# Kernel optimization log

Hardware: AMD Instinct MI355X
Metric: run time of the kernel (lower is better)

## Reference

```python
import jax, jax.numpy as jnp
import numpy as np

NEG_INF = -1e30


def setup_inputs() -> dict:
    key = jax.random.key(0)
    k1, k2, k3, k4, k5, k6 = jax.random.split(key, 6)
    T, B = 256, 8
    Din, Dm, A = 256, 256, 128
    input = jax.random.normal(k1, (T, B, Din), dtype=jnp.float32)
    memory = jax.random.normal(k2, (T, B, Dm), dtype=jnp.float32)
    memory_mask = jax.random.randint(k3, (T, B), 0, 2, dtype=jnp.int32)
    # first Linear weight [A, Din+Dm] split into input / memory halves (additive decomposition)
    scale1 = 1.0 / np.sqrt(Din + Dm)
    Wi = jax.random.uniform(k4, (Din, A), minval=-scale1, maxval=scale1, dtype=jnp.float32)
    Wm = jax.random.uniform(k5, (Dm, A), minval=-scale1, maxval=scale1, dtype=jnp.float32)
    # second Linear weight [1, A] -> vector [A]
    scale2 = 1.0 / np.sqrt(A)
    v = jax.random.uniform(k6, (A,), minval=-scale2, maxval=scale2, dtype=jnp.float32)
    return {"input": input, "memory": memory, "memory_mask": memory_mask,
            "Wi": Wi, "Wm": Wm, "v": v}


def reference(input, memory, memory_mask, Wi, Wm, v):
    # input: [T, B, Din], memory: [T, B, Dm], memory_mask: [T, B]
    # Additive (Bahdanau) scores: v . tanh(Wi x_s + Wm m_t). Concat+Linear on
    # [x; m] with block weight [Wi; Wm] equals the sum of the two projections.
    ip = jnp.einsum('tbd,da->tba', input, Wi)[:, None]    # [T, 1, B, A]
    mp = jnp.einsum('tbd,da->tba', memory, Wm)[None]      # [1, T, B, A]
    logits = jnp.einsum('stba,a->stb', jnp.tanh(ip + mp), v)  # [T, T, B]
    masked = jnp.where(memory_mask[None] != 0, logits, NEG_INF)
    score = jax.nn.softmax(masked, axis=1)                # softmax over key dim
    # NOTE: original module weights `input` (not memory) as values.
    context = jnp.einsum('stb,tbd->sbd', score, input)    # [T, B, Din]
    return jnp.concatenate([context, input], axis=-1)      # [T, B, 2*Din]
```

## Files before the change

### kernel.cpp

```cpp
#include <hip/hip_runtime.h>

#define T_DIM 256
#define B_DIM 8
#define DIN   256
#define DM    256
#define A_DIM 128
#define S_TILE 4
#define NEG_INF_F (-1e30f)

__global__ __launch_bounds__(256) void proj_kernel(
    const float* __restrict__ input, const float* __restrict__ memory,
    const float* __restrict__ Wi, const float* __restrict__ Wm,
    float* __restrict__ IP, float* __restrict__ MPt)
{
    __shared__ float xin[DIN];
    __shared__ float xmem[DM];
    const int tb  = blockIdx.x;
    const int t   = tb / B_DIM;
    const int b   = tb % B_DIM;
    const int tid = threadIdx.x;

    xin[tid]  = input[(t * B_DIM + b) * DIN + tid];
    xmem[tid] = memory[(t * B_DIM + b) * DM + tid];
    __syncthreads();

    if (tid < A_DIM) {
        const int a = tid;
        float acc = 0.f;
        #pragma unroll 8
        for (int d = 0; d < DIN; ++d)
            acc = fmaf(xin[d], Wi[d * A_DIM + a], acc);
        IP[(t * B_DIM + b) * A_DIM + a] = acc;
    } else {
        const int a = tid - A_DIM;
        float acc = 0.f;
        #pragma unroll 8
        for (int d = 0; d < DM; ++d)
            acc = fmaf(xmem[d], Wm[d * A_DIM + a], acc);
        MPt[(b * A_DIM + a) * T_DIM + t] = acc;
    }
}

__device__ inline float warp_red_max(float v) {
    #pragma unroll
    for (int o = 32; o > 0; o >>= 1) v = fmaxf(v, __shfl_xor(v, o, 64));
    return v;
}
__device__ inline float warp_red_sum(float v) {
    #pragma unroll
    for (int o = 32; o > 0; o >>= 1) v += __shfl_xor(v, o, 64);
    return v;
}

__global__ __launch_bounds__(256) void attn_kernel(
    const float* __restrict__ input, const int* __restrict__ mask,
    const float* __restrict__ v, const float* __restrict__ IP,
    const float* __restrict__ MPt, float* __restrict__ out)
{
    __shared__ float ip_s[S_TILE][A_DIM];
    __shared__ float vs[A_DIM];
    __shared__ float sc[S_TILE][T_DIM];
    __shared__ float red[4];

    const int blk = blockIdx.x;
    const int b   = blk % B_DIM;
    const int s0  = (blk / B_DIM) * S_TILE;
    const int tid = threadIdx.x;
    const int lane = tid & 63;
    const int wave = tid >> 6;

    if (tid < A_DIM) vs[tid] = v[tid];
    for (int i = tid; i < S_TILE * A_DIM; i += 256) {
        const int s = i / A_DIM, a = i % A_DIM;
        ip_s[s][a] = IP[((s0 + s) * B_DIM + b) * A_DIM + a];
    }
    __syncthreads();

    const int t = tid;
    float acc[S_TILE];
    #pragma unroll
    for (int s = 0; s < S_TILE; ++s) acc[s] = 0.f;

    const float* mp_base = MPt + (size_t)(b * A_DIM) * T_DIM + t;
    #pragma unroll 4
    for (int a = 0; a < A_DIM; ++a) {
        const float mp = mp_base[(size_t)a * T_DIM];
        const float va = vs[a];
        #pragma unroll
        for (int s = 0; s < S_TILE; ++s) {
            const float x = ip_s[s][a] + mp;
            const float e  = __expf(2.f * x);
            const float th = fmaf(-2.f, __builtin_amdgcn_rcpf(e + 1.f), 1.f);
            acc[s] = fmaf(va, th, acc[s]);
        }
    }

    const bool valid = (mask[t * B_DIM + b] != 0);

    #pragma unroll
    for (int s = 0; s < S_TILE; ++s) {
        const float masked = valid ? acc[s] : NEG_INF_F;
        float wm = warp_red_max(masked);
        if (lane == 0) red[wave] = wm;
        __syncthreads();
        const float m = fmaxf(fmaxf(red[0], red[1]), fmaxf(red[2], red[3]));
        const float e = __expf(masked - m);
        float ws = warp_red_sum(e);
        __syncthreads();
        if (lane == 0) red[wave] = ws;
        __syncthreads();
        const float sum = red[0] + red[1] + red[2] + red[3];
        sc[s][t] = e * __builtin_amdgcn_rcpf(sum);
        __syncthreads();
    }

    const int d = tid;
    float ctx[S_TILE];
    #pragma unroll
    for (int s = 0; s < S_TILE; ++s) ctx[s] = 0.f;

    #pragma unroll 4
    for (int t2 = 0; t2 < T_DIM; ++t2) {
        const float xv = input[(t2 * B_DIM + b) * DIN + d];
        #pragma unroll
        for (int s = 0; s < S_TILE; ++s)
            ctx[s] = fmaf(sc[s][t2], xv, ctx[s]);
    }

    #pragma unroll
    for (int s = 0; s < S_TILE; ++s) {
        const int srow = s0 + s;
        out[((size_t)(srow * B_DIM + b)) * (2 * DIN) + d]       = ctx[s];
        out[((size_t)(srow * B_DIM + b)) * (2 * DIN) + DIN + d] = input[(srow * B_DIM + b) * DIN + d];
    }
}

extern "C" void kernel_launch(void* const* d_in, const int* in_sizes, int n_in,
                              void* d_out, int out_size, void* d_ws, size_t ws_size,
                              hipStream_t stream) {
    const float* input  = (const float*)d_in[0];
    const float* memory = (const float*)d_in[1];
    const int*   mask   = (const int*)d_in[2];
    const float* Wi     = (const float*)d_in[3];
    const float* Wm     = (const float*)d_in[4];
    const float* v      = (const float*)d_in[5];
    float* out = (float*)d_out;

    float* IP  = (float*)d_ws;
    float* MPt = IP + (size_t)T_DIM * B_DIM * A_DIM;

    proj_kernel<<<T_DIM * B_DIM, 256, 0, stream>>>(input, memory, Wi, Wm, IP, MPt);
    attn_kernel<<<(T_DIM / S_TILE) * B_DIM, 256, 0, stream>>>(input, mask, v, IP, MPt, out);
}
```

Measured before the change: 116.4 us.

## Fold tanh scaling into projections and halve query tile

Pre-scales both projections by 2*log2(e) so the inner loop computes tanh through a raw exp2 and a reciprocal. The tanh constant terms are folded out of the loop: the sum of v times one is a per-row constant that cancels in the softmax, and the factor -2 is applied once to the logits. S_TILE drops from 4 to 2, which doubles the block count and merges the per-row softmax reductions into fewer barriers. The cost is twice as many reads of MPt and input across blocks, plus some change in float rounding.

```diff
diff --git a/kernel.cpp b/kernel.cpp
--- a/kernel.cpp
+++ b/kernel.cpp
@@ -5,8 +5,9 @@
 #define DIN   256
 #define DM    256
 #define A_DIM 128
-#define S_TILE 4
+#define S_TILE 2
 #define NEG_INF_F (-1e30f)
+#define PRESCALE 2.885390081777927f
 
 __global__ __launch_bounds__(256) void proj_kernel(
     const float* __restrict__ input, const float* __restrict__ memory,
@@ -30,14 +31,14 @@
         #pragma unroll 8
         for (int d = 0; d < DIN; ++d)
             acc = fmaf(xin[d], Wi[d * A_DIM + a], acc);
-        IP[(t * B_DIM + b) * A_DIM + a] = acc;
+        IP[(t * B_DIM + b) * A_DIM + a] = acc * PRESCALE;
     } else {
         const int a = tid - A_DIM;
         float acc = 0.f;
         #pragma unroll 8
         for (int d = 0; d < DM; ++d)
             acc = fmaf(xmem[d], Wm[d * A_DIM + a], acc);
-        MPt[(b * A_DIM + a) * T_DIM + t] = acc;
+        MPt[(b * A_DIM + a) * T_DIM + t] = acc * PRESCALE;
     }
 }
 
@@ -60,7 +61,7 @@
     __shared__ float ip_s[S_TILE][A_DIM];
     __shared__ float vs[A_DIM];
     __shared__ float sc[S_TILE][T_DIM];
-    __shared__ float red[4];
+    __shared__ float redm[S_TILE][4];
 
     const int blk = blockIdx.x;
     const int b   = blk % B_DIM;
@@ -77,61 +78,56 @@
     __syncthreads();
 
     const int t = tid;
-    float acc[S_TILE];
-    #pragma unroll
-    for (int s = 0; s < S_TILE; ++s) acc[s] = 0.f;
-
+    float acc0 = 0.f, acc1 = 0.f;
     const float* mp_base = MPt + (size_t)(b * A_DIM) * T_DIM + t;
-    #pragma unroll 4
+    #pragma unroll 8
     for (int a = 0; a < A_DIM; ++a) {
         const float mp = mp_base[(size_t)a * T_DIM];
         const float va = vs[a];
-        #pragma unroll
-        for (int s = 0; s < S_TILE; ++s) {
-            const float x = ip_s[s][a] + mp;
-            const float e  = __expf(2.f * x);
-            const float th = fmaf(-2.f, __builtin_amdgcn_rcpf(e + 1.f), 1.f);
-            acc[s] = fmaf(va, th, acc[s]);
-        }
+        const float e0 = __builtin_amdgcn_exp2f(ip_s[0][a] + mp);
+        const float e1 = __builtin_amdgcn_exp2f(ip_s[1][a] + mp);
+        acc0 = fmaf(va, __builtin_amdgcn_rcpf(e0 + 1.f), acc0);
+        acc1 = fmaf(va, __builtin_amdgcn_rcpf(e1 + 1.f), acc1);
     }
 
     const bool valid = (mask[t * B_DIM + b] != 0);
+    const float l0 = valid ? (-2.f * acc0) : NEG_INF_F;
+    const float l1 = valid ? (-2.f * acc1) : NEG_INF_F;
 
-    #pragma unroll
-    for (int s = 0; s < S_TILE; ++s) {
-        const float masked = valid ? acc[s] : NEG_INF_F;
-        float wm = warp_red_max(masked);
-        if (lane == 0) red[wave] = wm;
-        __syncthreads();
-        const float m = fmaxf(fmaxf(red[0], red[1]), fmaxf(red[2], red[3]));
-        const float e = __expf(masked - m);
-        float ws = warp_red_sum(e);
-        __syncthreads();
-        if (lane == 0) red[wave] = ws;
-        __syncthreads();
-        const float sum = red[0] + red[1] + red[2] + red[3];
-        sc[s][t] = e * __builtin_amdgcn_rcpf(sum);
-        __syncthreads();
+    float m0 = warp_red_max(l0), m1 = warp_red_max(l1);
+    if (lane == 0) { redm[0][wave] = m0; redm[1][wave] = m1; }
+    __syncthreads();
+    m0 = fmaxf(fmaxf(redm[0][0], redm[0][1]), fmaxf(redm[0][2], redm[0][3]));
+    m1 = fmaxf(fmaxf(redm[1][0], redm[1][1]), fmaxf(redm[1][2], redm[1][3]));
+    const float e0 = __expf(l0 - m0);
+    const float e1 = __expf(l1 - m1);
+    float su0 = warp_red_sum(e0), su1 = warp_red_sum(e1);
+    __syncthreads();
+    if (lane == 0) { redm[0][wave] = su0; redm[1][wave] = su1; }
+    __syncthreads();
+    su0 = (redm[0][0] + redm[0][1]) + (redm[0][2] + redm[0][3]);
+    su1 = (redm[1][0] + redm[1][1]) + (redm[1][2] + redm[1][3]);
+    sc[0][t] = e0 * __builtin_amdgcn_rcpf(su0);
+    sc[1][t] = e1 * __builtin_amdgcn_rcpf(su1);
+    __syncthreads();
+
+    const int d = tid;
+    float c0 = 0.f, c1 = 0.f;
+    const float* in_b = input + b * DIN + d;
+    #pragma unroll 8
+    for (int t2 = 0; t2 < T_DIM; ++t2) {
+        const float xv = in_b[(size_t)t2 * B_DIM * DIN];
+        c0 = fmaf(sc[0][t2], xv, c0);
+        c1 = fmaf(sc[1][t2], xv, c1);
     }
 
-    const int d = tid;
-    float ctx[S_TILE];
-    #pragma unroll
-    for (int s = 0; s < S_TILE; ++s) ctx[s] = 0.f;
-
-    #pragma unroll 4
-    for (int t2 = 0; t2 < T_DIM; ++t2) {
-        const float xv = input[(t2 * B_DIM + b) * DIN + d];
-        #pragma unroll
-        for (int s = 0; s < S_TILE; ++s)
-            ctx[s] = fmaf(sc[s][t2], xv, ctx[s]);
-    }
-
-    #pragma unroll
-    for (int s = 0; s < S_TILE; ++s) {
-        const int srow = s0 + s;
-        out[((size_t)(srow * B_DIM + b)) * (2 * DIN) + d]       = ctx[s];
-        out[((size_t)(srow * B_DIM + b)) * (2 * DIN) + DIN + d] = input[(srow * B_DIM + b) * DIN + d];
+    {
+        const int r0 = (s0 + 0) * B_DIM + b;
+        const int r1 = (s0 + 1) * B_DIM + b;
+        out[(size_t)r0 * (2 * DIN) + d]        = c0;
+        out[(size_t)r0 * (2 * DIN) + DIN + d]  = input[r0 * DIN + d];
+        out[(size_t)r1 * (2 * DIN) + d]        = c1;
+        out[(size_t)r1 * (2 * DIN) + DIN + d]  = input[r1 * DIN + d];
     }
 }
 
```

Measured after the change: 110.8 us. -4.8%, faster.

## Split attention into logits and context kernels, prescale projections for exp2 tanh

Applied to the files above, without the earlier changes.

Projections are prescaled by 2/ln2 so the tanh inner loop needs only an exp2 plus a reciprocal, with the affine tanh terms folded into the softmax logit as -2*acc (the constant drops out of softmax). The attention kernel is split into a per-query logits/softmax kernel with many more blocks and a separate context kernel that reads scores from workspace. The projection kernel now processes 4 rows per block to reuse weight loads. This adds an extra launch and a global round trip for the score matrix.

```diff
diff --git a/kernel.cpp b/kernel.cpp
--- a/kernel.cpp
+++ b/kernel.cpp
@@ -5,39 +5,56 @@
 #define DIN   256
 #define DM    256
 #define A_DIM 128
-#define S_TILE 4
 #define NEG_INF_F (-1e30f)
+#define PRESCALE 2.885390081777927f
+#define PROJ_TT 4
+#define CTX_ST  4
 
 __global__ __launch_bounds__(256) void proj_kernel(
     const float* __restrict__ input, const float* __restrict__ memory,
     const float* __restrict__ Wi, const float* __restrict__ Wm,
     float* __restrict__ IP, float* __restrict__ MPt)
 {
-    __shared__ float xin[DIN];
-    __shared__ float xmem[DM];
-    const int tb  = blockIdx.x;
-    const int t   = tb / B_DIM;
-    const int b   = tb % B_DIM;
-    const int tid = threadIdx.x;
+    __shared__ float xin[PROJ_TT][DIN];
+    __shared__ float xmem[PROJ_TT][DM];
+    const int row0 = blockIdx.x * PROJ_TT;
+    const int tid  = threadIdx.x;
 
-    xin[tid]  = input[(t * B_DIM + b) * DIN + tid];
-    xmem[tid] = memory[(t * B_DIM + b) * DM + tid];
+    #pragma unroll
+    for (int r = 0; r < PROJ_TT; ++r) {
+        xin[r][tid]  = input[(row0 + r) * DIN + tid];
+        xmem[r][tid] = memory[(row0 + r) * DM + tid];
+    }
     __syncthreads();
 
     if (tid < A_DIM) {
         const int a = tid;
-        float acc = 0.f;
+        float acc[PROJ_TT] = {0.f, 0.f, 0.f, 0.f};
         #pragma unroll 8
-        for (int d = 0; d < DIN; ++d)
-            acc = fmaf(xin[d], Wi[d * A_DIM + a], acc);
-        IP[(t * B_DIM + b) * A_DIM + a] = acc;
+        for (int d = 0; d < DIN; ++d) {
+            const float w = Wi[d * A_DIM + a];
+            #pragma unroll
+            for (int r = 0; r < PROJ_TT; ++r)
+                acc[r] = fmaf(xin[r][d], w, acc[r]);
+        }
+        #pragma unroll
+        for (int r = 0; r < PROJ_TT; ++r)
+            IP[(row0 + r) * A_DIM + a] = acc[r] * PRESCALE;
     } else {
         const int a = tid - A_DIM;
-        float acc = 0.f;
+        float acc[PROJ_TT] = {0.f, 0.f, 0.f, 0.f};
         #pragma unroll 8
-        for (int d = 0; d < DM; ++d)
-            acc = fmaf(xmem[d], Wm[d * A_DIM + a], acc);
-        MPt[(b * A_DIM + a) * T_DIM + t] = acc;
+        for (int d = 0; d < DM; ++d) {
+            const float w = Wm[d * A_DIM + a];
+            #pragma unroll
+            for (int r = 0; r < PROJ_TT; ++r)
+                acc[r] = fmaf(xmem[r][d], w, acc[r]);
+        }
+        #pragma unroll
+        for (int r = 0; r < PROJ_TT; ++r) {
+            const int t = (row0 + r) / B_DIM, b = (row0 + r) % B_DIM;
+            MPt[(b * A_DIM + a) * T_DIM + t] = acc[r] * PRESCALE;
+        }
     }
 }
 
@@ -52,86 +69,86 @@
     return v;
 }
 
-__global__ __launch_bounds__(256) void attn_kernel(
-    const float* __restrict__ input, const int* __restrict__ mask,
-    const float* __restrict__ v, const float* __restrict__ IP,
-    const float* __restrict__ MPt, float* __restrict__ out)
+__global__ __launch_bounds__(256) void logits_kernel(
+    const int* __restrict__ mask, const float* __restrict__ v,
+    const float* __restrict__ IP, const float* __restrict__ MPt,
+    float* __restrict__ SC)
 {
-    __shared__ float ip_s[S_TILE][A_DIM];
+    __shared__ float ip_s[A_DIM];
     __shared__ float vs[A_DIM];
-    __shared__ float sc[S_TILE][T_DIM];
     __shared__ float red[4];
 
     const int blk = blockIdx.x;
     const int b   = blk % B_DIM;
-    const int s0  = (blk / B_DIM) * S_TILE;
+    const int s   = blk / B_DIM;
     const int tid = threadIdx.x;
     const int lane = tid & 63;
     const int wave = tid >> 6;
 
-    if (tid < A_DIM) vs[tid] = v[tid];
-    for (int i = tid; i < S_TILE * A_DIM; i += 256) {
-        const int s = i / A_DIM, a = i % A_DIM;
-        ip_s[s][a] = IP[((s0 + s) * B_DIM + b) * A_DIM + a];
+    if (tid < A_DIM) {
+        vs[tid]   = v[tid];
+        ip_s[tid] = IP[(s * B_DIM + b) * A_DIM + tid];
     }
     __syncthreads();
 
     const int t = tid;
-    float acc[S_TILE];
-    #pragma unroll
-    for (int s = 0; s < S_TILE; ++s) acc[s] = 0.f;
-
+    float acc = 0.f;
     const float* mp_base = MPt + (size_t)(b * A_DIM) * T_DIM + t;
-    #pragma unroll 4
+    #pragma unroll 8
     for (int a = 0; a < A_DIM; ++a) {
         const float mp = mp_base[(size_t)a * T_DIM];
-        const float va = vs[a];
-        #pragma unroll
-        for (int s = 0; s < S_TILE; ++s) {
-            const float x = ip_s[s][a] + mp;
-            const float e  = __expf(2.f * x);
-            const float th = fmaf(-2.f, __builtin_amdgcn_rcpf(e + 1.f), 1.f);
-            acc[s] = fmaf(va, th, acc[s]);
-        }
+        const float e  = __builtin_amdgcn_exp2f(ip_s[a] + mp);
+        acc = fmaf(vs[a], __builtin_amdgcn_rcpf(e + 1.f), acc);
     }
 
     const bool valid = (mask[t * B_DIM + b] != 0);
+    const float l = valid ? (-2.f * acc) : NEG_INF_F;
 
-    #pragma unroll
-    for (int s = 0; s < S_TILE; ++s) {
-        const float masked = valid ? acc[s] : NEG_INF_F;
-        float wm = warp_red_max(masked);
-        if (lane == 0) red[wave] = wm;
-        __syncthreads();
-        const float m = fmaxf(fmaxf(red[0], red[1]), fmaxf(red[2], red[3]));
-        const float e = __expf(masked - m);
-        float ws = warp_red_sum(e);
-        __syncthreads();
-        if (lane == 0) red[wave] = ws;
-        __syncthreads();
-        const float sum = red[0] + red[1] + red[2] + red[3];
-        sc[s][t] = e * __builtin_amdgcn_rcpf(sum);
-        __syncthreads();
+    float m = warp_red_max(l);
+    if (lane == 0) red[wave] = m;
+    __syncthreads();
+    m = fmaxf(fmaxf(red[0], red[1]), fmaxf(red[2], red[3]));
+    const float e = __expf(l - m);
+    float su = warp_red_sum(e);
+    __syncthreads();
+    if (lane == 0) red[wave] = su;
+    __syncthreads();
+    su = (red[0] + red[1]) + (red[2] + red[3]);
+    SC[(s * B_DIM + b) * T_DIM + t] = e * __builtin_amdgcn_rcpf(su);
+}
+
+__global__ __launch_bounds__(256) void context_kernel(
+    const float* __restrict__ input, const float* __restrict__ SC,
+    float* __restrict__ out)
+{
+    __shared__ float sc_s[CTX_ST][T_DIM];
+    const int blk = blockIdx.x;
+    const int b   = blk % B_DIM;
+    const int s0  = (blk / B_DIM) * CTX_ST;
+    const int tid = threadIdx.x;
+
+    for (int i = tid; i < CTX_ST * T_DIM; i += 256) {
+        const int r = i >> 8, t = i & (T_DIM - 1);
+        sc_s[r][t] = SC[((s0 + r) * B_DIM + b) * T_DIM + t];
     }
+    __syncthreads();
 
     const int d = tid;
-    float ctx[S_TILE];
-    #pragma unroll
-    for (int s = 0; s < S_TILE; ++s) ctx[s] = 0.f;
-
-    #pragma unroll 4
+    float c[CTX_ST] = {0.f, 0.f, 0.f, 0.f};
+    const float* in_b = input + b * DIN + d;
+    #pragma unroll 8
     for (int t2 = 0; t2 < T_DIM; ++t2) {
-        const float xv = input[(t2 * B_DIM + b) * DIN + d];
+        const float xv = in_b[(size_t)t2 * B_DIM * DIN];
         #pragma unroll
-        for (int s = 0; s < S_TILE; ++s)
-            ctx[s] = fmaf(sc[s][t2], xv, ctx[s]);
+        for (int r = 0; r < CTX_ST; ++r)
+            c[r] = fmaf(sc_s[r][t2], xv, c[r]);
     }
 
     #pragma unroll
-    for (int s = 0; s < S_TILE; ++s) {
-        const int srow = s0 + s;
-        out[((size_t)(srow * B_DIM + b)) * (2 * DIN) + d]       = ctx[s];
-        out[((size_t)(srow * B_DIM + b)) * (2 * DIN) + DIN + d] = input[(srow * B_DIM + b) * DIN + d];
+    for (int r = 0; r < CTX_ST; ++r) {
+        const int row = (s0 + r) * B_DIM + b;
+        out[(size_t)row * (2 * DIN) + d]       = c[r];
+        out[(size_t)row * (2 * DIN) + DIN + d] = input[row * DIN + d];
     }
 }
 
@@ -147,8 +164,10 @@
     float* out = (float*)d_out;
 
     float* IP  = (float*)d_ws;
-    float* MPt = IP + (size_t)T_DIM * B_DIM * A_DIM;
+    float* MPt = IP  + (size_t)T_DIM * B_DIM * A_DIM;
+    float* SC  = MPt + (size_t)B_DIM * A_DIM * T_DIM;
 
-    proj_kernel<<<T_DIM * B_DIM, 256, 0, stream>>>(input, memory, Wi, Wm, IP, MPt);
-    attn_kernel<<<(T_DIM / S_TILE) * B_DIM, 256, 0, stream>>>(input, mask, v, IP, MPt, out);
+    proj_kernel<<<(T_DIM * B_DIM) / PROJ_TT, 256, 0, stream>>>(input, memory, Wi, Wm, IP, MPt);
+    logits_kernel<<<T_DIM * B_DIM, 256, 0, stream>>>(mask, v, IP, MPt, SC);
+    context_kernel<<<(T_DIM / CTX_ST) * B_DIM, 256, 0, stream>>>(input, SC, out);
 }
```

Result: faster. 111.1 us (-4.5%).
